# Optimization experiments

Measured on AMD Instinct MI355X. Metric: run time of the kernel, lower is better.

Reference implementation:

```python
import jax, jax.numpy as jnp
import numpy as np

N_NODES = 50000      # nodes
N_EDGES = 800000     # directed edges (avg degree 16)
HIDDEN = 128
F_IN = 11            # QM9 num_node_features
NUM_CLASSES = 19     # QM9 num targets
NUM_GRAPHS = 2048


def _glorot(key, fan_in, fan_out):
    lim = np.sqrt(6.0 / (fan_in + fan_out)).astype(np.float32)
    return jax.random.uniform(key, (fan_in, fan_out), jnp.float32, -lim, lim)


def setup_inputs() -> dict:
    key = jax.random.key(0)
    ks = jax.random.split(key, 8)
    x = jax.random.normal(ks[0], (N_NODES, F_IN), jnp.float32)
    edge_index = jax.random.randint(ks[1], (2, N_EDGES), 0, N_NODES, dtype=jnp.int64)
    batch = jnp.sort(jax.random.randint(ks[2], (N_NODES,), 0, NUM_GRAPHS, dtype=jnp.int64))
    W1 = _glorot(ks[3], F_IN, HIDDEN); b1 = jnp.zeros((HIDDEN,), jnp.float32)
    W2 = _glorot(ks[4], HIDDEN, HIDDEN); b2 = jnp.zeros((HIDDEN,), jnp.float32)
    W3 = _glorot(ks[5], HIDDEN, HIDDEN); b3 = jnp.zeros((HIDDEN,), jnp.float32)
    Wl = _glorot(ks[6], HIDDEN, NUM_CLASSES); bl = jnp.zeros((NUM_CLASSES,), jnp.float32)
    return dict(x=x, edge_index=edge_index, batch=batch,
                W1=W1, b1=b1, W2=W2, b2=b2, W3=W3, b3=b3, Wl=Wl, bl=bl)


def gcn_conv(x, src, dst, W, b, n):
    """PyG GCNConv: x' = D^-1/2 (A + I) D^-1/2 (x W) + b, degrees include self-loops."""
    h = x @ W                                                      # [n, out]
    deg = jax.ops.segment_sum(jnp.ones_like(dst, h.dtype), dst, num_segments=n) + 1.0
    dinv = jax.lax.rsqrt(deg)                                      # [n]
    norm = dinv[src] * dinv[dst]                                   # [E]
    agg = jax.ops.segment_sum(h[src] * norm[:, None], dst, num_segments=n)
    agg = agg + h * (dinv * dinv)[:, None]                         # self-loop term
    return agg + b


def reference(x, edge_index, batch, W1, b1, W2, b2, W3, b3, Wl, bl):
    src, dst = edge_index[0], edge_index[1]
    h = jax.nn.relu(gcn_conv(x, src, dst, W1, b1, N_NODES))
    h = jax.nn.relu(gcn_conv(h, src, dst, W2, b2, N_NODES))
    h = gcn_conv(h, src, dst, W3, b3, N_NODES)
    # global_mean_pool over graph ids
    sums = jax.ops.segment_sum(h, batch, num_segments=NUM_GRAPHS)
    cnt = jax.ops.segment_sum(jnp.ones((N_NODES,), h.dtype), batch, num_segments=NUM_GRAPHS)
    pooled = sums / jnp.maximum(cnt, 1.0)[:, None]                 # [G, H]
    # dropout is identity in eval mode
    return pooled @ Wl + bl                                        # [G, NUM_CLASSES]
```

## Files before the change

### kernel.cpp

```cpp
#include <hip/hip_runtime.h>
#include <hip/hip_bf16.h>
#include <hip/hip_fp16.h>


#define HIDDEN 128
#define F_IN 11
#define NCLS 19
#define NBITS 8
#define NB 256
#define RNODES 256
#define EPB 4096
#define OUTL_CAP 5376

typedef _Float16 half8 __attribute__((ext_vector_type(8)));
typedef float floatx4 __attribute__((ext_vector_type(4)));


__global__ void scatter_kernel(const int* __restrict__ src, const int* __restrict__ dst,
                               int* __restrict__ bcur, unsigned int* __restrict__ bents,
                               int E, int cap, int nSB,
                               const float* __restrict__ W3, const float* __restrict__ Wl,
                               const float* __restrict__ b3, float* __restrict__ W3l,
                               float* __restrict__ b3l, const float* __restrict__ W2,
                               __half* __restrict__ W2Th) {
    __shared__ int hist[NB];
    __shared__ int binoff[NB];
    __shared__ int runrel[NB];
    __shared__ unsigned int ebuf[EPB];
    __shared__ unsigned short binOf[EPB];
    __shared__ int cw[4];
    int tid = threadIdx.x, lane = tid & 63, w = tid >> 6;

    if (blockIdx.x >= nSB) {
        int xb = blockIdx.x - nSB;
        if (xb < 11) {
            float* Wls = (float*)ebuf;
            for (int i = tid; i < HIDDEN * NCLS; i += 256) Wls[i] = Wl[i];
            __syncthreads();
            if (xb < 10) {
                int o = xb * 256 + tid;
                if (o < HIDDEN * NCLS) {
                    int i = o / NCLS, j = o % NCLS;
                    float acc = 0.f;
#pragma unroll 8
                    for (int k = 0; k < HIDDEN; ++k) acc += W3[i * HIDDEN + k] * Wls[k * NCLS + j];
                    W3l[o] = acc;
                }
            } else if (tid < NCLS) {
                float acc = 0.f;
#pragma unroll 8
                for (int k = 0; k < HIDDEN; ++k) acc += b3[k] * Wls[k * NCLS + tid];
                b3l[tid] = acc;
            }
        } else {
            int base = (xb - 11) * 4096;
#pragma unroll
            for (int r = 0; r < 16; ++r) {
                int idx = base + tid + 256 * r;
                int k = idx >> 7, nn2 = idx & 127;
                W2Th[nn2 * HIDDEN + k] = __float2half(W2[idx]);
            }
        }
        return;
    }

    int base = blockIdx.x * EPB;
    int cnt = min(EPB, E - base);
    for (int i = tid; i < NB; i += 256) hist[i] = 0;
    __syncthreads();
    unsigned int pk[16];
    int rk[16];
#pragma unroll
    for (int j = 0; j < 16; ++j) {
        int idx = tid + 256 * j;
        if (idx < cnt) {
            int e = base + idx;
            int s = src[e], d = dst[e];
            pk[j] = (unsigned int)s | ((unsigned int)d << 16);
            int bin = d >> NBITS;
            int r = atomicAdd(&hist[bin], 1);
            rk[j] = r | (bin << 16);
        } else rk[j] = -1;
    }
    __syncthreads();
    int v = hist[tid], xv = v;
#pragma unroll
    for (int d = 1; d < 64; d <<= 1) {
        int t = __shfl_up(xv, d, 64);
        if (lane >= d) xv += t;
    }
    if (lane == 63) cw[w] = xv;
    __syncthreads();
    int waveoff = 0;
    for (int wi = 0; wi < w; ++wi) waveoff += cw[wi];
    binoff[tid] = waveoff + xv - v;
    runrel[tid] = v ? atomicAdd(&bcur[tid], v) : 0;
    __syncthreads();
#pragma unroll
    for (int j = 0; j < 16; ++j) {
        if (rk[j] >= 0) {
            int bin = rk[j] >> 16, r = rk[j] & 0xFFFF;
            int pos = binoff[bin] + r;
            ebuf[pos] = pk[j];
            binOf[pos] = (unsigned short)bin;
        }
    }
    __syncthreads();
    for (int i = tid; i < cnt; i += 256) {
        int bin = binOf[i];
        int rel = runrel[bin] + (i - binoff[bin]);
        if (rel < cap)
            bents[bin * cap + rel] = ebuf[i];
    }
}

__global__ void build_kernel(const unsigned int* __restrict__ bents, const int* __restrict__ bcur,
                             const float* __restrict__ x, const int* __restrict__ batch,
                             int2* __restrict__ begend, unsigned short* __restrict__ csr16,
                             float* __restrict__ dinv, float* __restrict__ gcnt,
                             __half* __restrict__ x16h, int n, int cap, int rst) {
    __shared__ int counts[RNODES];
    __shared__ int lcur[RNODES];
    __shared__ unsigned short outl[OUTL_CAP];
    __shared__ int wsums[4];
    int tid = threadIdx.x;
    int lane = tid & 63, w = tid >> 6;
    int b = blockIdx.x;
    int base = b << NBITS;
    int nn = min(RNODES, n - base);
    int ebase = b * cap;
    int ecnt = min(bcur[b], cap);
    int st = b * rst;
    for (int i = tid; i < RNODES; i += 512) counts[i] = 0;
    __syncthreads();
    for (int e = tid; e < ecnt; e += 512)
        atomicAdd(&counts[(bents[ebase + e] >> 16) - base], 1);
    __syncthreads();
    int v = 0, xv = 0;
    if (tid < RNODES) {
        v = (tid < nn) ? counts[tid] + 1 : 0;
        xv = v;
#pragma unroll
        for (int d = 1; d < 64; d <<= 1) {
            int t = __shfl_up(xv, d, 64);
            if (lane >= d) xv += t;
        }
        if (lane == 63) wsums[w] = xv;
    }
    __syncthreads();
    if (tid < nn) {
        int waveoff = 0;
        for (int wi = 0; wi < w; ++wi) waveoff += wsums[wi];
        int excl = waveoff + xv - v;
        lcur[tid] = excl + 1;
        outl[excl] = (unsigned short)(base + tid);
        begend[base + tid] = make_int2(st + excl, st + excl + v);
        atomicAdd(&gcnt[batch[base + tid]], 1.0f);
    }
    __syncthreads();
    for (int e = tid; e < ecnt; e += 512) {
        unsigned int pk = bents[ebase + e];
        int i = (int)(pk >> 16) - base;
        int r = atomicAdd(&lcur[i], 1);
        outl[r] = (unsigned short)(pk & 0xFFFFu);
    }
    __syncthreads();
    int total = ecnt + nn;
    for (int i = tid; i < total; i += 512)
        csr16[st + i] = outl[i];
    for (int idx = tid; idx < nn * 16; idx += 512) {
        int i = idx >> 4, j = idx & 15;
        float di = 1.0f / sqrtf((float)(counts[i] + 1));
        if (j == 0) dinv[base + i] = di;
        float xv2 = (j < F_IN) ? x[(long)(base + i) * F_IN + j] * di : 0.f;
        x16h[(long)(base + i) * 16 + j] = __float2half(xv2);
    }
}


__global__ void agg16_gemm_kernel(const __half* __restrict__ x16h, const int2* __restrict__ begend,
                                  const unsigned short* __restrict__ csr16,
                                  const float* __restrict__ dinv, const float* __restrict__ W1,
                                  const float* __restrict__ b1, __half* __restrict__ h1h, int n) {
    __shared__ float2 W1s[F_IN][64];
    __shared__ float2 bs[64];
    int tid = threadIdx.x;
    for (int i = tid; i < F_IN * 64; i += 256) {
        int k = i >> 6, j = i & 63;
        W1s[k][j] = make_float2(W1[k * HIDDEN + 2 * j], W1[k * HIDDEN + 2 * j + 1]);
    }
    if (tid < 64) bs[tid] = make_float2(b1[2 * tid], b1[2 * tid + 1]);
    __syncthreads();
    int node = (int)(((long)blockIdx.x * blockDim.x + threadIdx.x) >> 6);
    int lane = threadIdx.x & 63;
    if (node >= n) return;
    int grp = lane >> 4, f = lane & 15;
    int2 be = begend[node];
    int beg = be.x, end = be.y;
    float acc = 0.f;
    int eb = beg;
    for (; eb + 16 <= end; eb += 16) {
        int s[4]; __half v[4];
#pragma unroll
        for (int j = 0; j < 4; ++j) s[j] = csr16[eb + grp + 4 * j];
#pragma unroll
        for (int j = 0; j < 4; ++j) v[j] = x16h[(long)s[j] * 16 + f];
#pragma unroll
        for (int j = 0; j < 4; ++j) acc += __half2float(v[j]);
    }
    if (eb + 8 <= end) {
        int s0 = csr16[eb + grp], s1 = csr16[eb + grp + 4];
        acc += __half2float(x16h[(long)s0 * 16 + f]) + __half2float(x16h[(long)s1 * 16 + f]);
        eb += 8;
    }
    for (int e = eb + grp; e < end; e += 4)
        acc += __half2float(x16h[(long)csr16[e] * 16 + f]);
    acc += __shfl_down(acc, 32);
    acc += __shfl_down(acc, 16);
    float z = acc * dinv[node];
    float2 o = bs[lane];
#pragma unroll
    for (int k = 0; k < F_IN; ++k) {
        float zk = __shfl(z, k);
        float2 w = W1s[k][lane];
        o.x += zk * w.x;
        o.y += zk * w.y;
    }
    __half2 h = __floats2half2_rn(fmaxf(o.x, 0.f), fmaxf(o.y, 0.f));
    ((__half2*)h1h)[(long)node * 64 + lane] = h;
}


__global__ __launch_bounds__(256) void gemm_mfma_kernel(
        const __half* __restrict__ h1h, const __half* __restrict__ W2Th,
        const float* __restrict__ dinv, __half* __restrict__ hsh, int n) {
    __shared__ _Float16 W2T[128 * 136];
    __shared__ _Float16 outs[64 * 136];
    int tid = threadIdx.x;
    for (int i = tid; i < 128 * 16; i += 256) {
        int r = i >> 4, q = i & 15;
        *(uint4*)&W2T[r * 136 + q * 8] = ((const uint4*)W2Th)[r * 16 + q];
    }
    int base = blockIdx.x * 64;
    int lane = tid & 63, wid = tid >> 6;
    int l15 = lane & 15, quad = lane >> 4;
    int arow = base + wid * 16 + l15;
    if (arow >= n) arow = n - 1;
    const _Float16* Aptr = (const _Float16*)h1h + (size_t)arow * 128;
    floatx4 acc[8];
#pragma unroll
    for (int t = 0; t < 8; ++t) acc[t] = (floatx4){0.f, 0.f, 0.f, 0.f};
    __syncthreads();
#pragma unroll
    for (int c = 0; c < 4; ++c) {
        half8 a = *(const half8*)(Aptr + c * 32 + quad * 8);
#pragma unroll
        for (int t = 0; t < 8; ++t) {
            half8 b = *(const half8*)(&W2T[(t * 16 + l15) * 136 + c * 32 + quad * 8]);
            acc[t] = __builtin_amdgcn_mfma_f32_16x16x32_f16(a, b, acc[t], 0, 0, 0);
        }
    }
    float dv[4];
#pragma unroll
    for (int r = 0; r < 4; ++r) {
        int nd = base + wid * 16 + quad * 4 + r;
        dv[r] = dinv[(nd < n) ? nd : 0];
    }
#pragma unroll
    for (int t = 0; t < 8; ++t)
#pragma unroll
        for (int r = 0; r < 4; ++r)
            outs[(wid * 16 + quad * 4 + r) * 136 + t * 16 + l15] = (_Float16)(acc[t][r] * dv[r]);
    __syncthreads();
    for (int i = tid; i < 64 * 16; i += 256) {
        int ln = i >> 4, qq = i & 15;
        long nd = base + ln;
        if (nd < n) {
            uint4 u = *(uint4*)&outs[ln * 136 + qq * 8];
            ((uint4*)hsh)[nd * 16 + qq] = u;
        }
    }
}


__global__ void agg128h_kernel(const __half* __restrict__ hsh, const int2* __restrict__ begend,
                               const unsigned short* __restrict__ csr16, const float* __restrict__ dinv,
                               const float* __restrict__ bias, __half* __restrict__ outh, int n) {
    int node = (int)(((long)blockIdx.x * blockDim.x + threadIdx.x) >> 6);
    int lane = threadIdx.x & 63;
    if (node >= n) return;
    int grp = lane >> 5, q = lane & 31;
    int2 be = begend[node];
    int beg = be.x, end = be.y;
    float4 acc = make_float4(0.f, 0.f, 0.f, 0.f);
    int eb = beg;
    for (; eb + 16 <= end; eb += 16) {
        int s[8]; uint2 u[8];
#pragma unroll
        for (int j = 0; j < 8; ++j) s[j] = csr16[eb + grp + 2 * j];
#pragma unroll
        for (int j = 0; j < 8; ++j) u[j] = ((const uint2*)hsh)[(long)s[j] * 32 + q];
#pragma unroll
        for (int j = 0; j < 8; ++j) {
            float2 lo = __half22float2(*(__half2*)&u[j].x);
            float2 hi = __half22float2(*(__half2*)&u[j].y);
            acc.x += lo.x; acc.y += lo.y; acc.z += hi.x; acc.w += hi.y;
        }
    }
    if (eb + 8 <= end) {
        int s[4]; uint2 u[4];
#pragma unroll
        for (int j = 0; j < 4; ++j) s[j] = csr16[eb + grp + 2 * j];
#pragma unroll
        for (int j = 0; j < 4; ++j) u[j] = ((const uint2*)hsh)[(long)s[j] * 32 + q];
#pragma unroll
        for (int j = 0; j < 4; ++j) {
            float2 lo = __half22float2(*(__half2*)&u[j].x);
            float2 hi = __half22float2(*(__half2*)&u[j].y);
            acc.x += lo.x; acc.y += lo.y; acc.z += hi.x; acc.w += hi.y;
        }
        eb += 8;
    }
    for (int e = eb + grp; e < end; e += 2) {
        uint2 u = ((const uint2*)hsh)[(long)csr16[e] * 32 + q];
        float2 lo = __half22float2(*(__half2*)&u.x);
        float2 hi = __half22float2(*(__half2*)&u.y);
        acc.x += lo.x; acc.y += lo.y; acc.z += hi.x; acc.w += hi.y;
    }
    acc.x += __shfl_down(acc.x, 32);
    acc.y += __shfl_down(acc.y, 32);
    acc.z += __shfl_down(acc.z, 32);
    acc.w += __shfl_down(acc.w, 32);
    if (grp == 0) {
        float di = dinv[node];
        float4 b = ((const float4*)bias)[q];
        __half2 h01 = __floats2half2_rn(fmaxf(acc.x * di + b.x, 0.f), fmaxf(acc.y * di + b.y, 0.f));
        __half2 h23 = __floats2half2_rn(fmaxf(acc.z * di + b.z, 0.f), fmaxf(acc.w * di + b.w, 0.f));
        uint2 u = make_uint2(*(unsigned int*)&h01, *(unsigned int*)&h23);
        ((uint2*)outh)[(long)node * 32 + q] = u;
    }
}


__global__ void gemm_y32h_kernel(const __half* __restrict__ h2h, const float* __restrict__ W3l,
                                 const float* __restrict__ dinv, __half* __restrict__ ys, int n) {
    __shared__ float hs[12][HIDDEN];
    __shared__ float Ws[HIDDEN][20];
    int tid = threadIdx.x;
    long base = (long)blockIdx.x * 12;
    for (int i = tid; i < HIDDEN * NCLS; i += 256) Ws[i / NCLS][i % NCLS] = W3l[i];
    for (int idx = tid; idx < 12 * 32; idx += 256) {
        int node = idx >> 5, q = idx & 31;
        long gn = base + node;
        uint2 u = (gn < n) ? ((const uint2*)h2h)[gn * 32 + q] : make_uint2(0u, 0u);
        float2 lo = __half22float2(*(__half2*)&u.x);
        float2 hi = __half22float2(*(__half2*)&u.y);
        hs[node][q * 4] = lo.x; hs[node][q * 4 + 1] = lo.y;
        hs[node][q * 4 + 2] = hi.x; hs[node][q * 4 + 3] = hi.y;
    }
    __syncthreads();
    if (tid < 12 * NCLS) {
        int node = tid / NCLS, j = tid % NCLS;
        long gn = base + node;
        if (gn < n) {
            float acc = 0.f;
#pragma unroll 8
            for (int k = 0; k < HIDDEN; ++k) acc += hs[node][k] * Ws[k][j];
            ys[gn * 32 + j] = __float2half(acc * dinv[gn]);
        }
    }
    for (int idx = tid; idx < 12 * 13; idx += 256) {
        int node = idx / 13, j = 19 + idx % 13;
        long gn = base + node;
        if (gn < n) ys[gn * 32 + j] = __half(0.f);
    }
}

__global__ void agg24h_pool_kernel(const __half* __restrict__ ys, const int2* __restrict__ begend,
                                   const unsigned short* __restrict__ csr16, const float* __restrict__ dinv,
                                   const int* __restrict__ batch, float* __restrict__ pool, int n) {
    int node = (int)(((long)blockIdx.x * blockDim.x + threadIdx.x) >> 6);
    int lane = threadIdx.x & 63;
    if (node >= n) return;
    int grp = lane >> 4, f = lane & 15;
    int2 be = begend[node];
    int beg = be.x, end = be.y;
    float2 acc = {0.f, 0.f};
    int eb = beg;
    for (; eb + 32 <= end; eb += 32) {
        int s[8]; unsigned int u[8];
#pragma unroll
        for (int j = 0; j < 8; ++j) s[j] = csr16[eb + grp + 4 * j];
#pragma unroll
        for (int j = 0; j < 8; ++j) u[j] = ((const unsigned int*)ys)[(long)s[j] * 16 + f];
#pragma unroll
        for (int j = 0; j < 8; ++j) {
            float2 v = __half22float2(*(__half2*)&u[j]);
            acc.x += v.x; acc.y += v.y;
        }
    }
    if (eb + 16 <= end) {
        int s[4]; unsigned int u[4];
#pragma unroll
        for (int j = 0; j < 4; ++j) s[j] = csr16[eb + grp + 4 * j];
#pragma unroll
        for (int j = 0; j < 4; ++j) u[j] = ((const unsigned int*)ys)[(long)s[j] * 16 + f];
#pragma unroll
        for (int j = 0; j < 4; ++j) {
            float2 v = __half22float2(*(__half2*)&u[j]);
            acc.x += v.x; acc.y += v.y;
        }
        eb += 16;
    }
    for (int e = eb + grp; e < end; e += 4) {
        unsigned int u = ((const unsigned int*)ys)[(long)csr16[e] * 16 + f];
        float2 v = __half22float2(*(__half2*)&u);
        acc.x += v.x; acc.y += v.y;
    }
    acc.x += __shfl_down(acc.x, 32);
    acc.y += __shfl_down(acc.y, 32);
    acc.x += __shfl_down(acc.x, 16);
    acc.y += __shfl_down(acc.y, 16);
    if (lane < 16) {
        int g = batch[node];
        float sc = dinv[node];
        int c0 = 2 * f;
        if (c0 < NCLS) atomicAdd(&pool[(long)g * 24 + c0], acc.x * sc);
        if (c0 + 1 < NCLS) atomicAdd(&pool[(long)g * 24 + c0 + 1], acc.y * sc);
    }
}

__global__ void final_kernel(const float* __restrict__ pool, const float* __restrict__ cnt,
                             const float* __restrict__ b3l, const float* __restrict__ bl,
                             float* __restrict__ out, int G) {
    int i = blockIdx.x * blockDim.x + threadIdx.x;
    if (i >= G * NCLS) return;
    int g = i / NCLS, j = i % NCLS;
    float c = cnt[g];
    out[i] = (c > 0.f) ? pool[(long)g * 24 + j] / c + b3l[j] + bl[j] : bl[j];
}


static inline size_t align256(size_t x) { return (x + 255) & ~(size_t)255; }

extern "C" void kernel_launch(void* const* d_in, const int* in_sizes, int n_in,
                              void* d_out, int out_size, void* d_ws, size_t ws_size,
                              hipStream_t stream) {
    const float* x    = (const float*)d_in[0];
    const int*   ei   = (const int*)d_in[1];
    const int*   batch= (const int*)d_in[2];
    const float* W1   = (const float*)d_in[3];
    const float* b1   = (const float*)d_in[4];
    const float* W2   = (const float*)d_in[5];
    const float* b2   = (const float*)d_in[6];
    const float* W3   = (const float*)d_in[7];
    const float* b3   = (const float*)d_in[8];
    const float* Wl   = (const float*)d_in[9];
    const float* bl   = (const float*)d_in[10];
    float* out = (float*)d_out;

    const int N = in_sizes[0] / F_IN;
    const int E = in_sizes[1] / 2;
    const int G = out_size / NCLS;
    const int* src = ei;
    const int* dst = ei + E;
    const int nSB = (E + EPB - 1) / EPB;
    const int nBK = (N + RNODES - 1) / RNODES;
    int cap = (int)((long long)E * RNODES / N) + 768;
    if (cap + RNODES > OUTL_CAP) cap = OUTL_CAP - RNODES;
    const int rst = cap + RNODES;

    char* p = (char*)d_ws;
    size_t off = 0;
    unsigned int*   bents  = (unsigned int*)(p + off);   off = align256(off + (size_t)NB * cap * 4);
    unsigned short* csr16  = (unsigned short*)(p + off); off = align256(off + (size_t)NB * rst * 2);
    int2*           begend = (int2*)(p + off);           off = align256(off + (size_t)N * 8);
    float*          dinv   = (float*)(p + off);          off = align256(off + (size_t)N * 4);
    __half*         x16h   = (__half*)(p + off);         off = align256(off + (size_t)N * 16 * 2);
    __half*         h1h    = (__half*)(p + off);         off = align256(off + (size_t)N * HIDDEN * 2);
    __half*         hsh    = (__half*)(p + off);         off = align256(off + (size_t)N * HIDDEN * 2);
    __half*         h2h    = (__half*)(p + off);         off = align256(off + (size_t)N * HIDDEN * 2);
    __half*         y32h   = (__half*)(p + off);         off = align256(off + (size_t)N * 32 * 2);
    __half*         W2Th   = (__half*)(p + off);         off = align256(off + (size_t)HIDDEN * HIDDEN * 2);
    float*          W3l    = (float*)(p + off);          off = align256(off + (size_t)HIDDEN * NCLS * 4);
    float*          b3l    = (float*)(p + off);          off = align256(off + (size_t)NCLS * 4);
    float*          pool   = (float*)(p + off);
    float*          gcnt   = pool + (size_t)G * 24;
    int*            bcur   = (int*)(pool + (size_t)G * 25);
    off = align256(off + (size_t)G * 25 * 4 + NB * 4);
    (void)ws_size; (void)n_in;

    hipMemsetAsync(pool, 0, (size_t)G * 25 * 4 + NB * 4, stream);

    scatter_kernel<<<nSB + 15, 256, 0, stream>>>(src, dst, bcur, bents, E, cap, nSB,
                                                 W3, Wl, b3, W3l, b3l, W2, W2Th);
    build_kernel<<<nBK, 512, 0, stream>>>(bents, bcur, x, batch, begend, csr16,
                                          dinv, gcnt, x16h, N, cap, rst);

    const int aggBlocks = (N + 3) / 4;

    agg16_gemm_kernel<<<aggBlocks, 256, 0, stream>>>(x16h, begend, csr16, dinv, W1, b1, h1h, N);

    gemm_mfma_kernel<<<(N + 63) / 64, 256, 0, stream>>>(h1h, W2Th, dinv, hsh, N);
    agg128h_kernel<<<aggBlocks, 256, 0, stream>>>(hsh, begend, csr16, dinv, b2, h2h, N);

    gemm_y32h_kernel<<<(N + 11) / 12, 256, 0, stream>>>(h2h, W3l, dinv, y32h, N);
    agg24h_pool_kernel<<<aggBlocks, 256, 0, stream>>>(y32h, begend, csr16, dinv, batch, pool, N);
    final_kernel<<<(G * NCLS + 255) / 256, 256, 0, stream>>>(pool, gcnt, b3l, bl, out, G);
}
```

Before: 231.9 us.

## Fuse layer-2 aggregation with W3·Wl projection into one kernel

After: 233.5 us. No clear change (+0.7%).

```diff
diff --git a/kernel.cpp b/kernel.cpp
--- a/kernel.cpp
+++ b/kernel.cpp
@@ -283,98 +283,88 @@
 }
 
 
-__global__ void agg128h_kernel(const __half* __restrict__ hsh, const int2* __restrict__ begend,
-                               const unsigned short* __restrict__ csr16, const float* __restrict__ dinv,
-                               const float* __restrict__ bias, __half* __restrict__ outh, int n) {
-    int node = (int)(((long)blockIdx.x * blockDim.x + threadIdx.x) >> 6);
-    int lane = threadIdx.x & 63;
-    if (node >= n) return;
+__global__ void agg128h_y_kernel(const __half* __restrict__ hsh, const int2* __restrict__ begend,
+                                 const unsigned short* __restrict__ csr16, const float* __restrict__ dinv,
+                                 const float* __restrict__ bias, const float* __restrict__ W3l,
+                                 __half* __restrict__ ys, int n) {
+    __shared__ float Ws[HIDDEN][20];
+    __shared__ float hs[4][HIDDEN];
+    int tid = threadIdx.x;
+    for (int i = tid; i < HIDDEN * NCLS; i += 256) Ws[i / NCLS][i % NCLS] = W3l[i];
+    __syncthreads();
+    int node = (int)(((long)blockIdx.x * blockDim.x + tid) >> 6);
+    int lane = tid & 63, w = tid >> 6;
+    bool active = node < n;
     int grp = lane >> 5, q = lane & 31;
-    int2 be = begend[node];
-    int beg = be.x, end = be.y;
+    float di = 0.f;
     float4 acc = make_float4(0.f, 0.f, 0.f, 0.f);
-    int eb = beg;
-    for (; eb + 16 <= end; eb += 16) {
-        int s[8]; uint2 u[8];
-#pragma unroll
-        for (int j = 0; j < 8; ++j) s[j] = csr16[eb + grp + 2 * j];
-#pragma unroll
-        for (int j = 0; j < 8; ++j) u[j] = ((const uint2*)hsh)[(long)s[j] * 32 + q];
-#pragma unroll
-        for (int j = 0; j < 8; ++j) {
-            float2 lo = __half22float2(*(__half2*)&u[j].x);
-            float2 hi = __half22float2(*(__half2*)&u[j].y);
+    if (active) {
+        di = dinv[node];
+        int2 be = begend[node];
+        int beg = be.x, end = be.y;
+        int eb = beg;
+        for (; eb + 16 <= end; eb += 16) {
+            int s[8]; uint2 u[8];
+#pragma unroll
+            for (int j = 0; j < 8; ++j) s[j] = csr16[eb + grp + 2 * j];
+#pragma unroll
+            for (int j = 0; j < 8; ++j) u[j] = ((const uint2*)hsh)[(long)s[j] * 32 + q];
+#pragma unroll
+            for (int j = 0; j < 8; ++j) {
+                float2 lo = __half22float2(*(__half2*)&u[j].x);
+                float2 hi = __half22float2(*(__half2*)&u[j].y);
+                acc.x += lo.x; acc.y += lo.y; acc.z += hi.x; acc.w += hi.y;
+            }
+        }
+        if (eb + 8 <= end) {
+            int s[4]; uint2 u[4];
+#pragma unroll
+            for (int j = 0; j < 4; ++j) s[j] = csr16[eb + grp + 2 * j];
+#pragma unroll
+            for (int j = 0; j < 4; ++j) u[j] = ((const uint2*)hsh)[(long)s[j] * 32 + q];
+#pragma unroll
+            for (int j = 0; j < 4; ++j) {
+                float2 lo = __half22float2(*(__half2*)&u[j].x);
+                float2 hi = __half22float2(*(__half2*)&u[j].y);
+                acc.x += lo.x; acc.y += lo.y; acc.z += hi.x; acc.w += hi.y;
+            }
+            eb += 8;
+        }
+        for (int e = eb + grp; e < end; e += 2) {
+            uint2 u = ((const uint2*)hsh)[(long)csr16[e] * 32 + q];
+            float2 lo = __half22float2(*(__half2*)&u.x);
+            float2 hi = __half22float2(*(__half2*)&u.y);
             acc.x += lo.x; acc.y += lo.y; acc.z += hi.x; acc.w += hi.y;
         }
-    }
-    if (eb + 8 <= end) {
-        int s[4]; uint2 u[4];
-#pragma unroll
-        for (int j = 0; j < 4; ++j) s[j] = csr16[eb + grp + 2 * j];
-#pragma unroll
-        for (int j = 0; j < 4; ++j) u[j] = ((const uint2*)hsh)[(long)s[j] * 32 + q];
-#pragma unroll
-        for (int j = 0; j < 4; ++j) {
-            float2 lo = __half22float2(*(__half2*)&u[j].x);
-            float2 hi = __half22float2(*(__half2*)&u[j].y);
-            acc.x += lo.x; acc.y += lo.y; acc.z += hi.x; acc.w += hi.y;
-        }
-        eb += 8;
-    }
-    for (int e = eb + grp; e < end; e += 2) {
-        uint2 u = ((const uint2*)hsh)[(long)csr16[e] * 32 + q];
-        float2 lo = __half22float2(*(__half2*)&u.x);
-        float2 hi = __half22float2(*(__half2*)&u.y);
-        acc.x += lo.x; acc.y += lo.y; acc.z += hi.x; acc.w += hi.y;
-    }
-    acc.x += __shfl_down(acc.x, 32);
-    acc.y += __shfl_down(acc.y, 32);
-    acc.z += __shfl_down(acc.z, 32);
-    acc.w += __shfl_down(acc.w, 32);
-    if (grp == 0) {
-        float di = dinv[node];
-        float4 b = ((const float4*)bias)[q];
-        __half2 h01 = __floats2half2_rn(fmaxf(acc.x * di + b.x, 0.f), fmaxf(acc.y * di + b.y, 0.f));
-        __half2 h23 = __floats2half2_rn(fmaxf(acc.z * di + b.z, 0.f), fmaxf(acc.w * di + b.w, 0.f));
-        uint2 u = make_uint2(*(unsigned int*)&h01, *(unsigned int*)&h23);
-        ((uint2*)outh)[(long)node * 32 + q] = u;
-    }
-}
-
-
-__global__ void gemm_y32h_kernel(const __half* __restrict__ h2h, const float* __restrict__ W3l,
-                                 const float* __restrict__ dinv, __half* __restrict__ ys, int n) {
-    __shared__ float hs[12][HIDDEN];
-    __shared__ float Ws[HIDDEN][20];
-    int tid = threadIdx.x;
-    long base = (long)blockIdx.x * 12;
-    for (int i = tid; i < HIDDEN * NCLS; i += 256) Ws[i / NCLS][i % NCLS] = W3l[i];
-    for (int idx = tid; idx < 12 * 32; idx += 256) {
-        int node = idx >> 5, q = idx & 31;
-        long gn = base + node;
-        uint2 u = (gn < n) ? ((const uint2*)h2h)[gn * 32 + q] : make_uint2(0u, 0u);
-        float2 lo = __half22float2(*(__half2*)&u.x);
-        float2 hi = __half22float2(*(__half2*)&u.y);
-        hs[node][q * 4] = lo.x; hs[node][q * 4 + 1] = lo.y;
-        hs[node][q * 4 + 2] = hi.x; hs[node][q * 4 + 3] = hi.y;
-    }
-    __syncthreads();
-    if (tid < 12 * NCLS) {
-        int node = tid / NCLS, j = tid % NCLS;
-        long gn = base + node;
-        if (gn < n) {
-            float acc = 0.f;
+        acc.x += __shfl_down(acc.x, 32);
+        acc.y += __shfl_down(acc.y, 32);
+        acc.z += __shfl_down(acc.z, 32);
+        acc.w += __shfl_down(acc.w, 32);
+        if (grp == 0) {
+            float4 b = ((const float4*)bias)[q];
+            hs[w][q * 4 + 0] = fmaxf(acc.x * di + b.x, 0.f);
+            hs[w][q * 4 + 1] = fmaxf(acc.y * di + b.y, 0.f);
+            hs[w][q * 4 + 2] = fmaxf(acc.z * di + b.z, 0.f);
+            hs[w][q * 4 + 3] = fmaxf(acc.w * di + b.w, 0.f);
+        }
+    }
+    __syncthreads();
+    float yacc = 0.f;
+    int j = lane & 31;
+    int kbase = grp * 64;
+    if (j < NCLS) {
 #pragma unroll 8
-            for (int k = 0; k < HIDDEN; ++k) acc += hs[node][k] * Ws[k][j];
-            ys[gn * 32 + j] = __float2half(acc * dinv[gn]);
-        }
-    }
-    for (int idx = tid; idx < 12 * 13; idx += 256) {
-        int node = idx / 13, j = 19 + idx % 13;
-        long gn = base + node;
-        if (gn < n) ys[gn * 32 + j] = __half(0.f);
-    }
-}
+        for (int k = 0; k < 64; ++k) yacc += hs[w][kbase + k] * Ws[kbase + k][j];
+    }
+    yacc += __shfl_down(yacc, 32);
+    if (active) {
+        if (lane < NCLS)
+            ys[(long)node * 32 + lane] = __float2half(yacc * di);
+        else if (lane >= 32 && lane < 45)
+            ys[(long)node * 32 + (lane - 13)] = __half(0.f);
+    }
+}
+
 
 __global__ void agg24h_pool_kernel(const __half* __restrict__ ys, const int2* __restrict__ begend,
                                    const unsigned short* __restrict__ csr16, const float* __restrict__ dinv,
@@ -479,7 +469,6 @@
     __half*         x16h   = (__half*)(p + off);         off = align256(off + (size_t)N * 16 * 2);
     __half*         h1h    = (__half*)(p + off);         off = align256(off + (size_t)N * HIDDEN * 2);
     __half*         hsh    = (__half*)(p + off);         off = align256(off + (size_t)N * HIDDEN * 2);
-    __half*         h2h    = (__half*)(p + off);         off = align256(off + (size_t)N * HIDDEN * 2);
     __half*         y32h   = (__half*)(p + off);         off = align256(off + (size_t)N * 32 * 2);
     __half*         W2Th   = (__half*)(p + off);         off = align256(off + (size_t)HIDDEN * HIDDEN * 2);
     float*          W3l    = (float*)(p + off);          off = align256(off + (size_t)HIDDEN * NCLS * 4);
@@ -502,9 +491,9 @@
     agg16_gemm_kernel<<<aggBlocks, 256, 0, stream>>>(x16h, begend, csr16, dinv, W1, b1, h1h, N);
 
     gemm_mfma_kernel<<<(N + 63) / 64, 256, 0, stream>>>(h1h, W2Th, dinv, hsh, N);
-    agg128h_kernel<<<aggBlocks, 256, 0, stream>>>(hsh, begend, csr16, dinv, b2, h2h, N);
-
-    gemm_y32h_kernel<<<(N + 11) / 12, 256, 0, stream>>>(h2h, W3l, dinv, y32h, N);
+
+    agg128h_y_kernel<<<aggBlocks, 256, 0, stream>>>(hsh, begend, csr16, dinv, b2, W3l, y32h, N);
+
     agg24h_pool_kernel<<<aggBlocks, 256, 0, stream>>>(y32h, begend, csr16, dinv, batch, pool, N);
     final_kernel<<<(G * NCLS + 255) / 256, 256, 0, stream>>>(pool, gcnt, b3l, bl, out, G);
 }
```
